# Performance work log

Measured on AMD Instinct MI355X. Metric: run time of the kernel, lower is better.

## Reference

```python
import jax, jax.numpy as jnp
import numpy as np

N_NODES = 50000
N_EDGES = 800000
D_IN = 128
D_OUT = 128


def setup_inputs() -> dict:
    key = jax.random.key(0)
    k1, k2, k3, k4, k5 = jax.random.split(key, 5)
    H = jax.random.normal(k1, (N_NODES, D_IN), dtype=jnp.float32)
    stdv = 1.0 / np.sqrt(D_OUT)
    W = jax.random.uniform(k2, (D_IN, D_OUT), dtype=jnp.float32, minval=-stdv, maxval=stdv)
    bias = jnp.zeros((D_OUT,), dtype=jnp.float32)
    edge_vals = jax.random.uniform(k3, (N_EDGES,), dtype=jnp.float32)
    edge_rows = jax.random.randint(k4, (N_EDGES,), 0, N_NODES, dtype=jnp.int32)
    edge_cols = jax.random.randint(k5, (N_EDGES,), 0, N_NODES, dtype=jnp.int32)
    return {"H": H, "W": W, "bias": bias, "edge_vals": edge_vals,
            "edge_rows": edge_rows, "edge_cols": edge_cols}


def reference(H, W, bias, edge_vals, edge_rows, edge_cols):
    # H' = relu(A @ (H W) + b), A given as COO edge list (rows, cols, vals)
    n = H.shape[0]
    HW = H @ W  # [N, D_out]
    # SpMM: out[r] = sum_{e: row(e)=r} val(e) * HW[col(e)]
    msgs = edge_vals[:, None] * HW[edge_cols]  # [E, D_out]
    out = jax.ops.segment_sum(msgs, edge_rows, num_segments=n)
    out = out + bias
    return jax.nn.relu(out)
```

## Files before the change

kernel.cpp:

```cpp
#include <hip/hip_runtime.h>

#define D 128
#define BM 64
#define NBB 256
#define BINSH 6
#define MAXBINS 1024
#define CAPB 1536

typedef __attribute__((ext_vector_type(8))) short bf16x8;
typedef __attribute__((ext_vector_type(4))) float f32x4;

__device__ __forceinline__ unsigned short f2bf(float f) {
    unsigned u = __float_as_uint(f);
    u = (u + 0x7FFFu + ((u >> 16) & 1u)) >> 16;
    return (unsigned short)u;
}
__device__ __forceinline__ float bf2f(unsigned short h) {
    return __uint_as_float(((unsigned)h) << 16);
}

__global__ __launch_bounds__(128) void k_prepw(const float* __restrict__ W,
                                               unsigned short* __restrict__ Wt,
                                               int* __restrict__ gcnt, int nbins) {
    int nn = blockIdx.x, k = threadIdx.x;
    Wt[nn * D + k] = f2bf(W[k * D + nn]);
    int gtid = blockIdx.x * 128 + threadIdx.x;
    for (int i = gtid; i < nbins * 16; i += 128 * D) gcnt[i] = 0;
}

__global__ __launch_bounds__(256) void k_gemm_bin(const float* __restrict__ H,
                                                  const unsigned short* __restrict__ Wt,
                                                  unsigned short* __restrict__ HWb,
                                                  int n,
                                                  const int* __restrict__ rows,
                                                  const int* __restrict__ cols,
                                                  const float* __restrict__ vals,
                                                  int* __restrict__ gcnt,
                                                  int2* __restrict__ segs,
                                                  int E, int nbins, int nbb) {
    __shared__ unsigned short sA[BM * 64];
    __shared__ unsigned short sB[D * 64];
    const int tid = threadIdx.x;
    const int row0 = blockIdx.x * BM;
    const int w = tid >> 6, l = tid & 63;
    const int lr = l & 15, lq = l >> 4;

    f32x4 acc[8];
#pragma unroll
    for (int ct = 0; ct < 8; ++ct) acc[ct] = (f32x4){0.f, 0.f, 0.f, 0.f};

#pragma unroll
    for (int kt = 0; kt < 2; ++kt) {
        if (kt) __syncthreads();
#pragma unroll
        for (int s = 0; s < 4; ++s) {
            int idx = s * 256 + tid;
            int r = idx >> 3, cc = idx & 7;
            bf16x8 v = *reinterpret_cast<const bf16x8*>(&Wt[(size_t)r * D + kt * 64 + cc * 8]);
            *reinterpret_cast<bf16x8*>(&sB[r * 64 + ((cc ^ (r & 7)) * 8)]) = v;
        }
#pragma unroll
        for (int s = 0; s < 2; ++s) {
            int idx = s * 256 + tid;
            int r = idx >> 3, cc = idx & 7;
            int row = row0 + r;
            float4 u0 = make_float4(0.f, 0.f, 0.f, 0.f), u1 = u0;
            if (row < n) {
                const float4* p = reinterpret_cast<const float4*>(
                    &H[(size_t)row * D + kt * 64 + cc * 8]);
                u0 = p[0]; u1 = p[1];
            }
            bf16x8 v;
            v[0] = (short)f2bf(u0.x); v[1] = (short)f2bf(u0.y);
            v[2] = (short)f2bf(u0.z); v[3] = (short)f2bf(u0.w);
            v[4] = (short)f2bf(u1.x); v[5] = (short)f2bf(u1.y);
            v[6] = (short)f2bf(u1.z); v[7] = (short)f2bf(u1.w);
            *reinterpret_cast<bf16x8*>(&sA[r * 64 + ((cc ^ (r & 7)) * 8)]) = v;
        }
        __syncthreads();

#pragma unroll
        for (int ks = 0; ks < 2; ++ks) {
            const int arow = w * 16 + lr;
            const int acc_c = (ks * 4 + lq) ^ (arow & 7);
            bf16x8 a = *reinterpret_cast<const bf16x8*>(&sA[arow * 64 + acc_c * 8]);
#pragma unroll
            for (int ct = 0; ct < 8; ++ct) {
                const int brow = ct * 16 + lr;
                const int bcc = (ks * 4 + lq) ^ (brow & 7);
                bf16x8 b = *reinterpret_cast<const bf16x8*>(&sB[brow * 64 + bcc * 8]);
                acc[ct] = __builtin_amdgcn_mfma_f32_16x16x32_bf16(b, a, acc[ct], 0, 0, 0);
            }
        }
    }

    {
        int row = row0 + w * 16 + lr;
        if (row < n) {
#pragma unroll
            for (int ct = 0; ct < 8; ++ct) {
                ushort4 o;
                o.x = f2bf(acc[ct][0]); o.y = f2bf(acc[ct][1]);
                o.z = f2bf(acc[ct][2]); o.w = f2bf(acc[ct][3]);
                *reinterpret_cast<ushort4*>(&HWb[(size_t)row * D + ct * 16 + lq * 4]) = o;
            }
        }
    }

    if (blockIdx.x < (unsigned)nbb) {
        __syncthreads();
        int* lcnt = reinterpret_cast<int*>(sA);
        int* loff = lcnt + MAXBINS;
        int chunk = (E + nbb - 1) / nbb;
        int s = blockIdx.x * chunk;
        int epos = s + chunk; if (epos > E) epos = E;
        for (int i = tid; i < nbins; i += 256) lcnt[i] = 0;
        __syncthreads();
        for (int e = s + tid; e < epos; e += 256)
            atomicAdd(&lcnt[rows[e] >> BINSH], 1);
        __syncthreads();
        for (int i = tid; i < nbins; i += 256) {
            int c = lcnt[i];
            int base = c ? atomicAdd(&gcnt[i * 16], c) : 0;
            loff[i] = i * CAPB + base;
            lcnt[i] = 0;
        }
        __syncthreads();
        for (int e = s + tid; e < epos; e += 256) {
            int r = rows[e];
            int c = cols[e];
            float v = vals[e];
            int bin = r >> BINSH;
            int p = atomicAdd(&lcnt[bin], 1);
            int pos = loff[bin] + p;
            if (pos < (bin + 1) * CAPB)
                segs[pos] = make_int2(((r & 63) << 16) | c, __float_as_int(v));
        }
    }
}

__global__ __launch_bounds__(512) void k_spmm(const unsigned short* __restrict__ HWb,
                                              const int* __restrict__ gcnt,
                                              const int2* __restrict__ segs,
                                              const float* __restrict__ bias,
                                              float* __restrict__ out, int n) {
    __shared__ int2 sent[CAPB];
    __shared__ int lcnt[64];
    __shared__ int loff[64];
    __shared__ int lcur[64];
    const int b = blockIdx.x;
    int cnt = gcnt[b * 16];
    if (cnt > CAPB) cnt = CAPB;
    const int2* seg = segs + (size_t)b * CAPB;

    if (threadIdx.x < 64) lcnt[threadIdx.x] = 0;
    __syncthreads();
    int2 er[3];
#pragma unroll
    for (int k = 0; k < 3; ++k) {
        int i = threadIdx.x + k * 512;
        if (i < cnt) {
            er[k] = seg[i];
            atomicAdd(&lcnt[((unsigned)er[k].x) >> 16], 1);
        }
    }
    __syncthreads();
    if (threadIdx.x < 64) {
        int v = lcnt[threadIdx.x];
        int inc = v;
#pragma unroll
        for (int o = 1; o < 64; o <<= 1) {
            int t = __shfl_up(inc, o);
            if (threadIdx.x >= o) inc += t;
        }
        loff[threadIdx.x] = inc - v;
        lcur[threadIdx.x] = inc - v;
    }
    __syncthreads();
#pragma unroll
    for (int k = 0; k < 3; ++k) {
        int i = threadIdx.x + k * 512;
        if (i < cnt) {
            int p = atomicAdd(&lcur[((unsigned)er[k].x) >> 16], 1);
            sent[p] = er[k];
        }
    }
    __syncthreads();

    const int w = threadIdx.x >> 6, lane = threadIdx.x & 63;
    const unsigned c2 = 2 * lane;
    const float2 bb = *reinterpret_cast<const float2*>(&bias[c2]);

    for (int rr = w; rr < 64; rr += 8) {
        int row = b * 64 + rr;
        if (row >= n) break;
        int s = loff[rr];
        int deg = lcnt[rr];
        float a0 = 0.f, a1 = 0.f, b0 = 0.f, b1 = 0.f;
        int t = 0;
        for (; t + 8 <= deg; t += 8) {
            int2 e0 = sent[s + t],     e1 = sent[s + t + 1];
            int2 e2 = sent[s + t + 2], e3 = sent[s + t + 3];
            int2 e4 = sent[s + t + 4], e5 = sent[s + t + 5];
            int2 e6 = sent[s + t + 6], e7 = sent[s + t + 7];
            unsigned m0 = *reinterpret_cast<const unsigned*>(&HWb[(size_t)(e0.x & 0xFFFF) * D + c2]);
            unsigned m1 = *reinterpret_cast<const unsigned*>(&HWb[(size_t)(e1.x & 0xFFFF) * D + c2]);
            unsigned m2 = *reinterpret_cast<const unsigned*>(&HWb[(size_t)(e2.x & 0xFFFF) * D + c2]);
            unsigned m3 = *reinterpret_cast<const unsigned*>(&HWb[(size_t)(e3.x & 0xFFFF) * D + c2]);
            unsigned m4 = *reinterpret_cast<const unsigned*>(&HWb[(size_t)(e4.x & 0xFFFF) * D + c2]);
            unsigned m5 = *reinterpret_cast<const unsigned*>(&HWb[(size_t)(e5.x & 0xFFFF) * D + c2]);
            unsigned m6 = *reinterpret_cast<const unsigned*>(&HWb[(size_t)(e6.x & 0xFFFF) * D + c2]);
            unsigned m7 = *reinterpret_cast<const unsigned*>(&HWb[(size_t)(e7.x & 0xFFFF) * D + c2]);
            float v0 = __int_as_float(e0.y), v1 = __int_as_float(e1.y);
            float v2 = __int_as_float(e2.y), v3 = __int_as_float(e3.y);
            float v4 = __int_as_float(e4.y), v5 = __int_as_float(e5.y);
            float v6 = __int_as_float(e6.y), v7 = __int_as_float(e7.y);
            a0 += v0 * bf2f((unsigned short)(m0 & 0xFFFF));
            a1 += v0 * bf2f((unsigned short)(m0 >> 16));
            b0 += v1 * bf2f((unsigned short)(m1 & 0xFFFF));
            b1 += v1 * bf2f((unsigned short)(m1 >> 16));
            a0 += v2 * bf2f((unsigned short)(m2 & 0xFFFF));
            a1 += v2 * bf2f((unsigned short)(m2 >> 16));
            b0 += v3 * bf2f((unsigned short)(m3 & 0xFFFF));
            b1 += v3 * bf2f((unsigned short)(m3 >> 16));
            a0 += v4 * bf2f((unsigned short)(m4 & 0xFFFF));
            a1 += v4 * bf2f((unsigned short)(m4 >> 16));
            b0 += v5 * bf2f((unsigned short)(m5 & 0xFFFF));
            b1 += v5 * bf2f((unsigned short)(m5 >> 16));
            a0 += v6 * bf2f((unsigned short)(m6 & 0xFFFF));
            a1 += v6 * bf2f((unsigned short)(m6 >> 16));
            b0 += v7 * bf2f((unsigned short)(m7 & 0xFFFF));
            b1 += v7 * bf2f((unsigned short)(m7 >> 16));
        }
        for (; t < deg; ++t) {
            int2 e = sent[s + t];
            unsigned m = *reinterpret_cast<const unsigned*>(&HWb[(size_t)(e.x & 0xFFFF) * D + c2]);
            float v = __int_as_float(e.y);
            a0 += v * bf2f((unsigned short)(m & 0xFFFF));
            a1 += v * bf2f((unsigned short)(m >> 16));
        }
        float2 o;
        o.x = fmaxf(a0 + b0 + bb.x, 0.f);
        o.y = fmaxf(a1 + b1 + bb.y, 0.f);
        *reinterpret_cast<float2*>(&out[(size_t)row * D + c2]) = o;
    }
}

__global__ void k_init_bias(const float* __restrict__ bias, float* __restrict__ out, int n) {
    int i = blockIdx.x * blockDim.x + threadIdx.x;
    if (i < n * D) out[i] = bias[i & (D - 1)];
}
__global__ void k_scatter(const unsigned short* __restrict__ HWb, const int* __restrict__ rows,
                          const int* __restrict__ cols, const float* __restrict__ vals,
                          float* __restrict__ out, int E) {
    int e = blockIdx.x * 2 + (threadIdx.x >> 7);
    int j = threadIdx.x & (D - 1);
    if (e < E) {
        int r = rows[e];
        int c = cols[e];
        float v = vals[e];
        atomicAdd(&out[(size_t)r * D + j], v * bf2f(HWb[(size_t)c * D + j]));
    }
}
__global__ void k_relu(float* __restrict__ out, int n) {
    int i = blockIdx.x * blockDim.x + threadIdx.x;
    if (i < n * D) out[i] = fmaxf(out[i], 0.f);
}

extern "C" void kernel_launch(void* const* d_in, const int* in_sizes, int n_in,
                              void* d_out, int out_size, void* d_ws, size_t ws_size,
                              hipStream_t stream) {
    const float* H         = (const float*)d_in[0];
    const float* W         = (const float*)d_in[1];
    const float* bias      = (const float*)d_in[2];
    const float* edge_vals = (const float*)d_in[3];
    const int*   edge_rows = (const int*)d_in[4];
    const int*   edge_cols = (const int*)d_in[5];
    float* out = (float*)d_out;

    const int n = in_sizes[0] / D;
    const int E = in_sizes[3];
    const int gblocks = (n + BM - 1) / BM;
    const int nbins = (n + 63) >> BINSH;
    const int nbb = (gblocks < NBB) ? gblocks : NBB;

    char* ws = (char*)d_ws;
    unsigned short* HWb = (unsigned short*)ws; ws += (size_t)n * D * sizeof(unsigned short);
    unsigned short* Wt  = (unsigned short*)ws; ws += (size_t)D * D * sizeof(unsigned short);
    int* gcnt = (int*)ws;            ws += (size_t)nbins * 16 * sizeof(int);
    int2* segs = (int2*)ws;          ws += (size_t)nbins * CAPB * sizeof(int2);
    size_t need_full = (size_t)(ws - (char*)d_ws);

    k_prepw<<<D, D, 0, stream>>>(W, Wt, gcnt, nbins);

    if (ws_size >= need_full && n < 65536 && nbins <= MAXBINS) {
        k_gemm_bin<<<gblocks, 256, 0, stream>>>(H, Wt, HWb, n,
                                                edge_rows, edge_cols, edge_vals,
                                                gcnt, segs, E, nbins, nbb);
        k_spmm<<<nbins, 512, 0, stream>>>(HWb, gcnt, segs, bias, out, n);
    } else {
        k_gemm_bin<<<gblocks, 256, 0, stream>>>(H, Wt, HWb, n,
                                                edge_rows, edge_cols, edge_vals,
                                                (int*)d_ws, (int2*)d_ws, 0, nbins, 0);
        k_init_bias<<<((size_t)n * D + 255) / 256, 256, 0, stream>>>(bias, out, n);
        k_scatter<<<(E + 1) / 2, 256, 0, stream>>>(HWb, edge_rows, edge_cols, edge_vals, out, E);
        k_relu<<<((size_t)n * D + 255) / 256, 256, 0, stream>>>(out, n);
    }
}
```

Measured before the change: 74.43 us.

## Replace global-atomic edge binning with per-block local sort and offset table

Edge binning is split out of the GEMM kernel into its own kernel. Each of 512 blocks counting-sorts its chunk of edges by bin in shared memory and writes them contiguously, along with a per-block offset table. This removes the global atomics on per-bin counters and the zeroing of those counters. The SpMM kernel then gathers each bin's pieces from all 512 partitions using a prefix scan, which costs 512 scattered offset reads per bin, serial per-thread copy loops and an extra shared buffer. It also adds a kernel launch and gives up the overlap of binning with the GEMM.

New measurement: 69.34 us. 1.07x faster.

```diff
diff --git a/kernel.cpp b/kernel.cpp
--- a/kernel.cpp
+++ b/kernel.cpp
@@ -2,7 +2,7 @@
 
 #define D 128
 #define BM 64
-#define NBB 256
+#define NBS 512
 #define BINSH 6
 #define MAXBINS 1024
 #define CAPB 1536
@@ -20,24 +20,15 @@
 }
 
 __global__ __launch_bounds__(128) void k_prepw(const float* __restrict__ W,
-                                               unsigned short* __restrict__ Wt,
-                                               int* __restrict__ gcnt, int nbins) {
+                                               unsigned short* __restrict__ Wt) {
     int nn = blockIdx.x, k = threadIdx.x;
     Wt[nn * D + k] = f2bf(W[k * D + nn]);
-    int gtid = blockIdx.x * 128 + threadIdx.x;
-    for (int i = gtid; i < nbins * 16; i += 128 * D) gcnt[i] = 0;
-}
-
-__global__ __launch_bounds__(256) void k_gemm_bin(const float* __restrict__ H,
-                                                  const unsigned short* __restrict__ Wt,
-                                                  unsigned short* __restrict__ HWb,
-                                                  int n,
-                                                  const int* __restrict__ rows,
-                                                  const int* __restrict__ cols,
-                                                  const float* __restrict__ vals,
-                                                  int* __restrict__ gcnt,
-                                                  int2* __restrict__ segs,
-                                                  int E, int nbins, int nbb) {
+}
+
+__global__ __launch_bounds__(256) void k_gemm(const float* __restrict__ H,
+                                              const unsigned short* __restrict__ Wt,
+                                              unsigned short* __restrict__ HWb,
+                                              int n) {
     __shared__ unsigned short sA[BM * 64];
     __shared__ unsigned short sB[D * 64];
     const int tid = threadIdx.x;
@@ -94,100 +85,178 @@
         }
     }
 
+    int row = row0 + w * 16 + lr;
+    if (row < n) {
+#pragma unroll
+        for (int ct = 0; ct < 8; ++ct) {
+            ushort4 o;
+            o.x = f2bf(acc[ct][0]); o.y = f2bf(acc[ct][1]);
+            o.z = f2bf(acc[ct][2]); o.w = f2bf(acc[ct][3]);
+            *reinterpret_cast<ushort4*>(&HWb[(size_t)row * D + ct * 16 + lq * 4]) = o;
+        }
+    }
+}
+
+__global__ __launch_bounds__(256) void k_bsort(const int* __restrict__ rows,
+                                               const int* __restrict__ cols,
+                                               const float* __restrict__ vals,
+                                               int2* __restrict__ segs,
+                                               int* __restrict__ offt,
+                                               int E, int nbins, int chunk) {
+    __shared__ int hist[MAXBINS];
+    __shared__ int excl[MAXBINS + 1];
+    __shared__ int wsum[4];
+    __shared__ int2 ebuf[1600];
+    const int tid = threadIdx.x;
+    const int p = blockIdx.x;
+    const int s = p * chunk;
+    int epos = s + chunk; if (epos > E) epos = E;
+    const int len = (epos > s) ? (epos - s) : 0;
+
+    for (int i = tid; i < nbins; i += 256) hist[i] = 0;
+    __syncthreads();
+    if (len > 0) {
+        const int t0 = s + (len & ~3);
+        for (int base = s + tid * 4; base + 4 <= epos; base += 1024) {
+            int4 r4 = *reinterpret_cast<const int4*>(&rows[base]);
+            atomicAdd(&hist[r4.x >> BINSH], 1);
+            atomicAdd(&hist[r4.y >> BINSH], 1);
+            atomicAdd(&hist[r4.z >> BINSH], 1);
+            atomicAdd(&hist[r4.w >> BINSH], 1);
+        }
+        for (int e = t0 + tid; e < epos; e += 256)
+            atomicAdd(&hist[rows[e] >> BINSH], 1);
+    }
+    __syncthreads();
+
+    int b0 = tid * 4;
+    int h0 = 0, h1 = 0, h2 = 0, h3 = 0, sum = 0;
+    if (b0 < nbins) {
+        h0 = hist[b0];
+        h1 = (b0 + 1 < nbins) ? hist[b0 + 1] : 0;
+        h2 = (b0 + 2 < nbins) ? hist[b0 + 2] : 0;
+        h3 = (b0 + 3 < nbins) ? hist[b0 + 3] : 0;
+        sum = h0 + h1 + h2 + h3;
+    }
     {
-        int row = row0 + w * 16 + lr;
-        if (row < n) {
-#pragma unroll
-            for (int ct = 0; ct < 8; ++ct) {
-                ushort4 o;
-                o.x = f2bf(acc[ct][0]); o.y = f2bf(acc[ct][1]);
-                o.z = f2bf(acc[ct][2]); o.w = f2bf(acc[ct][3]);
-                *reinterpret_cast<ushort4*>(&HWb[(size_t)row * D + ct * 16 + lq * 4]) = o;
-            }
-        }
-    }
-
-    if (blockIdx.x < (unsigned)nbb) {
+        int lane = tid & 63, w = tid >> 6;
+        int inc = sum;
+#pragma unroll
+        for (int o = 1; o < 64; o <<= 1) {
+            int t = __shfl_up(inc, o);
+            if (lane >= o) inc += t;
+        }
+        if (lane == 63) wsum[w] = inc;
         __syncthreads();
-        int* lcnt = reinterpret_cast<int*>(sA);
-        int* loff = lcnt + MAXBINS;
-        int chunk = (E + nbb - 1) / nbb;
-        int s = blockIdx.x * chunk;
-        int epos = s + chunk; if (epos > E) epos = E;
-        for (int i = tid; i < nbins; i += 256) lcnt[i] = 0;
-        __syncthreads();
-        for (int e = s + tid; e < epos; e += 256)
-            atomicAdd(&lcnt[rows[e] >> BINSH], 1);
-        __syncthreads();
-        for (int i = tid; i < nbins; i += 256) {
-            int c = lcnt[i];
-            int base = c ? atomicAdd(&gcnt[i * 16], c) : 0;
-            loff[i] = i * CAPB + base;
-            lcnt[i] = 0;
-        }
-        __syncthreads();
-        for (int e = s + tid; e < epos; e += 256) {
+        int wex = 0;
+        for (int j = 0; j < w; ++j) wex += wsum[j];
+        int cur = wex + inc - sum;
+        if (b0 < nbins) {
+            excl[b0] = cur; hist[b0] = cur; cur += h0;
+            if (b0 + 1 < nbins) { excl[b0 + 1] = cur; hist[b0 + 1] = cur; cur += h1; }
+            if (b0 + 2 < nbins) { excl[b0 + 2] = cur; hist[b0 + 2] = cur; cur += h2; }
+            if (b0 + 3 < nbins) { excl[b0 + 3] = cur; hist[b0 + 3] = cur; cur += h3; }
+        }
+        if (tid == 255) excl[nbins] = len;
+    }
+    __syncthreads();
+
+    if (len > 0) {
+        const int t0 = s + (len & ~3);
+        for (int base = s + tid * 4; base + 4 <= epos; base += 1024) {
+            int4 r4 = *reinterpret_cast<const int4*>(&rows[base]);
+            int4 c4 = *reinterpret_cast<const int4*>(&cols[base]);
+            float4 v4 = *reinterpret_cast<const float4*>(&vals[base]);
+            int q0 = atomicAdd(&hist[r4.x >> BINSH], 1);
+            int q1 = atomicAdd(&hist[r4.y >> BINSH], 1);
+            int q2 = atomicAdd(&hist[r4.z >> BINSH], 1);
+            int q3 = atomicAdd(&hist[r4.w >> BINSH], 1);
+            ebuf[q0] = make_int2(((r4.x & 63) << 16) | c4.x, __float_as_int(v4.x));
+            ebuf[q1] = make_int2(((r4.y & 63) << 16) | c4.y, __float_as_int(v4.y));
+            ebuf[q2] = make_int2(((r4.z & 63) << 16) | c4.z, __float_as_int(v4.z));
+            ebuf[q3] = make_int2(((r4.w & 63) << 16) | c4.w, __float_as_int(v4.w));
+        }
+        for (int e = t0 + tid; e < epos; e += 256) {
             int r = rows[e];
-            int c = cols[e];
-            float v = vals[e];
-            int bin = r >> BINSH;
-            int p = atomicAdd(&lcnt[bin], 1);
-            int pos = loff[bin] + p;
-            if (pos < (bin + 1) * CAPB)
-                segs[pos] = make_int2(((r & 63) << 16) | c, __float_as_int(v));
-        }
-    }
+            int q = atomicAdd(&hist[r >> BINSH], 1);
+            ebuf[q] = make_int2(((r & 63) << 16) | cols[e], __float_as_int(vals[e]));
+        }
+    }
+    __syncthreads();
+
+    for (int i = tid; i < len; i += 256)
+        segs[(size_t)p * chunk + i] = ebuf[i];
+    const int NS = nbins + 1;
+    for (int i = tid; i <= nbins; i += 256)
+        offt[(size_t)p * NS + i] = p * chunk + excl[i];
 }
 
 __global__ __launch_bounds__(512) void k_spmm(const unsigned short* __restrict__ HWb,
-                                              const int* __restrict__ gcnt,
+                                              const int* __restrict__ offt,
                                               const int2* __restrict__ segs,
                                               const float* __restrict__ bias,
-                                              float* __restrict__ out, int n) {
+                                              float* __restrict__ out, int n, int nbins) {
+    __shared__ int2 ent[CAPB];
     __shared__ int2 sent[CAPB];
     __shared__ int lcnt[64];
     __shared__ int loff[64];
     __shared__ int lcur[64];
+    __shared__ int wsum[8];
+    __shared__ int total_s;
     const int b = blockIdx.x;
-    int cnt = gcnt[b * 16];
-    if (cnt > CAPB) cnt = CAPB;
-    const int2* seg = segs + (size_t)b * CAPB;
-
-    if (threadIdx.x < 64) lcnt[threadIdx.x] = 0;
-    __syncthreads();
-    int2 er[3];
-#pragma unroll
-    for (int k = 0; k < 3; ++k) {
-        int i = threadIdx.x + k * 512;
-        if (i < cnt) {
-            er[k] = seg[i];
-            atomicAdd(&lcnt[((unsigned)er[k].x) >> 16], 1);
-        }
-    }
-    __syncthreads();
-    if (threadIdx.x < 64) {
-        int v = lcnt[threadIdx.x];
-        int inc = v;
+    const int tid = threadIdx.x;
+    const int NS = nbins + 1;
+
+    int o0 = offt[(size_t)tid * NS + b];
+    int o1 = offt[(size_t)tid * NS + b + 1];
+    int c = o1 - o0;
+    {
+        int lane = tid & 63, w = tid >> 6;
+        int inc = c;
 #pragma unroll
         for (int o = 1; o < 64; o <<= 1) {
             int t = __shfl_up(inc, o);
-            if (threadIdx.x >= o) inc += t;
-        }
-        loff[threadIdx.x] = inc - v;
-        lcur[threadIdx.x] = inc - v;
-    }
-    __syncthreads();
-#pragma unroll
-    for (int k = 0; k < 3; ++k) {
-        int i = threadIdx.x + k * 512;
-        if (i < cnt) {
-            int p = atomicAdd(&lcur[((unsigned)er[k].x) >> 16], 1);
-            sent[p] = er[k];
-        }
-    }
-    __syncthreads();
-
-    const int w = threadIdx.x >> 6, lane = threadIdx.x & 63;
+            if (lane >= o) inc += t;
+        }
+        if (lane == 63) wsum[w] = inc;
+        __syncthreads();
+        int wex = 0;
+        for (int j = 0; j < w; ++j) wex += wsum[j];
+        int myoff = wex + inc - c;
+        if (tid == 511) total_s = wex + inc;
+        for (int j = 0; j < c; ++j) {
+            int q = myoff + j;
+            if (q < CAPB) ent[q] = segs[o0 + j];
+        }
+    }
+    if (tid < 64) lcnt[tid] = 0;
+    __syncthreads();
+    int cnt = total_s;
+    if (cnt > CAPB) cnt = CAPB;
+
+    for (int i = tid; i < cnt; i += 512)
+        atomicAdd(&lcnt[((unsigned)ent[i].x) >> 16], 1);
+    __syncthreads();
+    if (tid < 64) {
+        int v = lcnt[tid];
+        int inc = v;
+#pragma unroll
+        for (int o = 1; o < 64; o <<= 1) {
+            int t = __shfl_up(inc, o);
+            if (tid >= o) inc += t;
+        }
+        loff[tid] = inc - v;
+        lcur[tid] = inc - v;
+    }
+    __syncthreads();
+    for (int i = tid; i < cnt; i += 512) {
+        int2 e = ent[i];
+        int q = atomicAdd(&lcur[((unsigned)e.x) >> 16], 1);
+        sent[q] = e;
+    }
+    __syncthreads();
+
+    const int w = tid >> 6, lane = tid & 63;
     const unsigned c2 = 2 * lane;
     const float2 bb = *reinterpret_cast<const float2*>(&bias[c2]);
 
@@ -282,26 +351,24 @@
     const int E = in_sizes[3];
     const int gblocks = (n + BM - 1) / BM;
     const int nbins = (n + 63) >> BINSH;
-    const int nbb = (gblocks < NBB) ? gblocks : NBB;
+    int chunk = (E + NBS - 1) / NBS;
+    chunk = (chunk + 3) & ~3;
 
     char* ws = (char*)d_ws;
     unsigned short* HWb = (unsigned short*)ws; ws += (size_t)n * D * sizeof(unsigned short);
     unsigned short* Wt  = (unsigned short*)ws; ws += (size_t)D * D * sizeof(unsigned short);
-    int* gcnt = (int*)ws;            ws += (size_t)nbins * 16 * sizeof(int);
-    int2* segs = (int2*)ws;          ws += (size_t)nbins * CAPB * sizeof(int2);
+    int2* segs = (int2*)ws;          ws += (size_t)NBS * chunk * sizeof(int2);
+    int* offt  = (int*)ws;           ws += (size_t)NBS * (nbins + 1) * sizeof(int);
     size_t need_full = (size_t)(ws - (char*)d_ws);
 
-    k_prepw<<<D, D, 0, stream>>>(W, Wt, gcnt, nbins);
-
-    if (ws_size >= need_full && n < 65536 && nbins <= MAXBINS) {
-        k_gemm_bin<<<gblocks, 256, 0, stream>>>(H, Wt, HWb, n,
-                                                edge_rows, edge_cols, edge_vals,
-                                                gcnt, segs, E, nbins, nbb);
-        k_spmm<<<nbins, 512, 0, stream>>>(HWb, gcnt, segs, bias, out, n);
+    k_prepw<<<D, D, 0, stream>>>(W, Wt);
+    k_gemm<<<gblocks, 256, 0, stream>>>(H, Wt, HWb, n);
+
+    if (ws_size >= need_full && n < 65536 && nbins <= MAXBINS && chunk <= 1600) {
+        k_bsort<<<NBS, 256, 0, stream>>>(edge_rows, edge_cols, edge_vals,
+                                         segs, offt, E, nbins, chunk);
+        k_spmm<<<nbins, 512, 0, stream>>>(HWb, offt, segs, bias, out, n, nbins);
     } else {
-        k_gemm_bin<<<gblocks, 256, 0, stream>>>(H, Wt, HWb, n,
-                                                edge_rows, edge_cols, edge_vals,
-                                                (int*)d_ws, (int2*)d_ws, 0, nbins, 0);
         k_init_bias<<<((size_t)n * D + 255) / 256, 256, 0, stream>>>(bias, out, n);
         k_scatter<<<(E + 1) / 2, 256, 0, stream>>>(HWb, edge_rows, edge_cols, edge_vals, out, E);
         k_relu<<<((size_t)n * D + 255) / 256, 256, 0, stream>>>(out, n);
```
